# Kernel tuning notes

Measured on AMD Instinct MI355X. Metric: run time of the kernel, lower is better.

## Reference

```python
import jax, jax.numpy as jnp
import numpy as np

NUM_FEATURE = 50


def setup_inputs() -> dict:
    key = jax.random.key(0)
    k1, k2 = jax.random.split(key)
    query = jax.random.normal(k1, (512, NUM_FEATURE), dtype=jnp.float32)
    doc = jax.random.normal(k2, (512, 256, NUM_FEATURE), dtype=jnp.float32)
    # nn.Linear(150, 1, bias=False) with weight filled with 1
    W = jnp.ones((3 * NUM_FEATURE,), dtype=jnp.float32)
    return {"query": query, "doc": doc, "W": W}


def reference(query, doc, W):
    # Split the single 150-dim linear weight into the three trilinear parts:
    # score(x, y) = w1.sen_x + w2.q_y + w3.(sen_x * q_y)
    w1, w2, w3 = W[:NUM_FEATURE], W[NUM_FEATURE:2 * NUM_FEATURE], W[2 * NUM_FEATURE:]
    q_term = query @ w2                      # [Lq]
    qw3 = query * w3                         # [Lq, d]

    def per_sentence(sen):                   # sen: [Ls, d]
        sXY = (sen @ w1)[:, None] + q_term[None, :] + sen @ qw3.T   # [Ls, Lq]
        sD2Q = jax.nn.softmax(sXY, axis=0)   # softmax over sentence tokens
        sQ2D = jax.nn.softmax(sXY, axis=1)   # softmax over query tokens
        aD2Q = sD2Q @ query                  # [Ls, d]
        aQ2D = sD2Q @ (sQ2D.T @ sen)         # (sD2Q @ sQ2D.T) @ sen, cheaper order
        return jnp.concatenate([sen, aD2Q, sen * aD2Q, sen * aQ2D], axis=1)  # [Ls, 4d]

    return jax.vmap(per_sentence)(doc)       # [n_sen, Ls, 4d]
```

## Files before the change

### kernel.cpp

```cpp
#include <hip/hip_runtime.h>
#include <math.h>

typedef __bf16 bf16_t;
typedef bf16_t bf16x2 __attribute__((ext_vector_type(2)));
typedef bf16_t bf16x4 __attribute__((ext_vector_type(4)));
typedef bf16_t bf16x8 __attribute__((ext_vector_type(8)));
typedef float f32x4 __attribute__((ext_vector_type(4)));

#define MFMA16(a,b,c) __builtin_amdgcn_mfma_f32_16x16x32_bf16((a),(b),(c),0,0,0)

#define ND 256
#define NQ 512
#define NF 50
#define L2E 1.44269504f
#define SHIFT 64.0f

#define SENT_E 0
#define PD_E   13728
#define PQ_E   23968
#define QW3_E  32416
#define QTT_E  34720
#define GT_E   36800
#define SEN72_E 13728
#define P1Q_E  13728
#define PART_B 77760
#define QTB_B  78784
#define RINV_B 79808
#define LDS_BYTES 80832

__launch_bounds__(512, 4)
__global__ void ca15_kernel(const float* __restrict__ query,
                            const float* __restrict__ doc,
                            const float* __restrict__ W,
                            float* __restrict__ out)
{
    extern __shared__ char smem[];
    bf16_t* lb = (bf16_t*)smem;
    float*  part  = (float*)(smem + PART_B);
    bf16_t* qtb   = (bf16_t*)(smem + QTB_B);
    float*  rinvf = (float*)(smem + RINV_B);

    const int tid = threadIdx.x;
    const int w = tid >> 6, l = tid & 63, ln = l & 15, lg = l >> 4;
    const int s = blockIdx.x;
    const float* sen_g = doc + (size_t)s * (ND * NF);
    const bf16x4 z4 = (bf16x4){(bf16_t)0.f,(bf16_t)0.f,(bf16_t)0.f,(bf16_t)0.f};

    auto stage_p1 = [&](int jt, int buf) {
        const int j0 = jt * 64;
        bf16_t* dst = lb + P1Q_E + buf * 4608;
        for (int e = tid; e < 1664; e += 512) {
            int jj = e / 26, c = e - jj * 26;
            if (c < 25) {
                float2 v = ((const float2*)query)[(j0 + jj) * 25 + c];
                bf16x2 p;
                p[0] = (bf16_t)(v.x * W[100 + 2 * c] * L2E);
                p[1] = (bf16_t)(v.y * W[100 + 2 * c + 1] * L2E);
                *(bf16x2*)&dst[jj * 72 + 2 * c] = p;
            } else {
                bf16x2 p;
                p[0] = (bf16_t)((float)qtb[j0 + jj] * L2E);
                p[1] = (bf16_t)L2E;
                *(bf16x2*)&dst[jj * 72 + 50] = p;
            }
        }
    };
    auto stage_qw3 = [&](int jt) {
        const int j0 = jt * 32;
        bf16_t* dst = lb + QW3_E;
        for (int e = tid; e < 832; e += 512) {
            int jj = e / 26, c = e - jj * 26;
            if (c < 25) {
                float2 v = ((const float2*)query)[(j0 + jj) * 25 + c];
                bf16x2 p;
                p[0] = (bf16_t)(v.x * W[100 + 2 * c] * L2E);
                p[1] = (bf16_t)(v.y * W[100 + 2 * c + 1] * L2E);
                *(bf16x2*)&dst[jj * 72 + 2 * c] = p;
            } else {
                bf16x2 p;
                p[0] = (bf16_t)((float)qtb[j0 + jj] * L2E);
                p[1] = (bf16_t)L2E;
                *(bf16x2*)&dst[jj * 72 + 50] = p;
            }
        }
    };
    auto stage_qtt = [&](int jt) {
        const int j0 = jt * 32;
        for (int e = tid; e < 800; e += 512) {
            int c = e >> 5, jj = e & 31;
            float2 v = ((const float2*)query)[(j0 + jj) * 25 + c];
            lb[QTT_E + (2 * c) * 40 + jj]     = (bf16_t)v.x;
            lb[QTT_E + (2 * c + 1) * 40 + jj] = (bf16_t)v.y;
        }
    };

    for (int e = tid; e < 132; e += 512) {
        int f = 50 + e / 66, c4 = (e - (e / 66) * 66) * 4;
        *(bf16x4*)&lb[SENT_E + f * 264 + c4] = z4;
    }
    for (int e = tid; e < 768; e += 512) {
        int i = e / 3, c4 = 52 + (e - (e / 3) * 3) * 4;
        *(bf16x4*)&lb[SEN72_E + i * 72 + c4] = z4;
    }
    for (int e = tid; e < 6400; e += 512) {
        int i = e / 25, c = e - (e / 25) * 25;
        float2 v = ((const float2*)sen_g)[i * 25 + c];
        bf16x2 p; p[0] = (bf16_t)v.x; p[1] = (bf16_t)v.y;
        *(bf16x2*)&lb[SEN72_E + i * 72 + 2 * c] = p;
        lb[SENT_E + (2 * c) * 264 + i]     = p[0];
        lb[SENT_E + (2 * c + 1) * 264 + i] = p[1];
    }
    {
        float acc = 0.f;
        #pragma unroll
        for (int c = 0; c < 25; ++c) {
            float2 v = ((const float2*)query)[tid * 25 + c];
            acc += v.x * W[NF + 2 * c] + v.y * W[NF + 2 * c + 1];
        }
        qtb[tid] = (bf16_t)acc;
    }
    if (tid < ND) {
        float acc = 0.f;
        #pragma unroll
        for (int c = 0; c < 25; ++c) {
            float2 v = ((const float2*)sen_g)[tid * 25 + c];
            acc += v.x * W[2 * c] + v.y * W[2 * c + 1];
        }
        lb[SEN72_E + tid * 72 + 50] = (bf16_t)1.0f;
        lb[SEN72_E + tid * 72 + 51] = (bf16_t)acc;
    }
    __syncthreads();

    bf16x8 aS[2][2];
    #pragma unroll
    for (int mf = 0; mf < 2; ++mf)
        #pragma unroll
        for (int ks = 0; ks < 2; ++ks)
            aS[mf][ks] = *(bf16x8*)&lb[SEN72_E + (w * 32 + mf * 16 + ln) * 72 + lg * 8 + ks * 32];
    __syncthreads();

    for (int e = tid; e < 384; e += 512) {
        int buf = e / 192, r = e - buf * 192;
        int jj = r / 3, c4 = 52 + (r - (r / 3) * 3) * 4;
        *(bf16x4*)&lb[P1Q_E + buf * 4608 + jj * 72 + c4] = z4;
    }
    stage_p1(0, 0);
    __syncthreads();

    float rpart[2][4] = {{0.f,0.f,0.f,0.f},{0.f,0.f,0.f,0.f}};
    for (int jt = 0; jt < 8; ++jt) {
        if (jt < 7) stage_p1(jt + 1, (jt + 1) & 1);
        const bf16_t* qb = lb + P1Q_E + (jt & 1) * 4608;
        f32x4 sacc[2][4];
        #pragma unroll
        for (int mf = 0; mf < 2; ++mf)
            #pragma unroll
            for (int nf = 0; nf < 4; ++nf)
                sacc[mf][nf] = (f32x4){-SHIFT, -SHIFT, -SHIFT, -SHIFT};
        #pragma unroll
        for (int ks = 0; ks < 2; ++ks)
            #pragma unroll
            for (int nf = 0; nf < 4; ++nf) {
                bf16x8 b = *(bf16x8*)&qb[(nf * 16 + ln) * 72 + lg * 8 + ks * 32];
                sacc[0][nf] = MFMA16(aS[0][ks], b, sacc[0][nf]);
                sacc[1][nf] = MFMA16(aS[1][ks], b, sacc[1][nf]);
            }
        #pragma unroll
        for (int mf = 0; mf < 2; ++mf)
            #pragma unroll
            for (int nf = 0; nf < 4; ++nf)
                #pragma unroll
                for (int r = 0; r < 4; ++r)
                    rpart[mf][r] += exp2f(sacc[mf][nf][r]);
        __syncthreads();
    }
    #pragma unroll
    for (int mf = 0; mf < 2; ++mf)
        #pragma unroll
        for (int r = 0; r < 4; ++r) {
            float v = rpart[mf][r];
            v += __shfl_xor(v, 1);
            v += __shfl_xor(v, 2);
            v += __shfl_xor(v, 4);
            v += __shfl_xor(v, 8);
            if (ln == 0) rinvf[w * 32 + mf * 16 + lg * 4 + r] = 1.f / v;
        }
    __syncthreads();
    for (int e = tid; e < 12800; e += 512) {
        int f = e / 256, i = e & 255;
        lb[SENT_E + f * 264 + i] = (bf16_t)((float)lb[SENT_E + f * 264 + i] * rinvf[i]);
    }
    for (int e = tid; e < 96; e += 512) {
        int jj = e / 3, c4 = 52 + (e - (e / 3) * 3) * 4;
        *(bf16x4*)&lb[QW3_E + jj * 72 + c4] = z4;
    }
    stage_qw3(0);
    __syncthreads();

    f32x4 accD[2][4], accQ[2][4];
    #pragma unroll
    for (int mf = 0; mf < 2; ++mf)
        #pragma unroll
        for (int nf = 0; nf < 4; ++nf) {
            accD[mf][nf] = (f32x4){0.f, 0.f, 0.f, 0.f};
            accQ[mf][nf] = (f32x4){0.f, 0.f, 0.f, 0.f};
        }
    bf16x8 aPs[2];
    const int jf = w & 1, ff = w >> 1;
    int qtt_row[4], gt_row[4];
    #pragma unroll
    for (int nf = 0; nf < 4; ++nf) {
        int f = nf * 16 + ln;
        int rc = f < 51 ? f : 51;
        qtt_row[nf] = QTT_E + rc * 40;
        gt_row[nf]  = GT_E + rc * 40;
    }
    const int fg = ff * 16 + ln;
    const int sent_row = SENT_E + (fg < 51 ? fg : 51) * 264;

    for (int jt = 0; jt < 16; ++jt) {
        if (jt > 0) {
            #pragma unroll
            for (int nf = 0; nf < 4; ++nf) {
                bf16x8 bg = *(bf16x8*)&lb[gt_row[nf] + lg * 8];
                accQ[0][nf] = MFMA16(aPs[0], bg, accQ[0][nf]);
                accQ[1][nf] = MFMA16(aPs[1], bg, accQ[1][nf]);
            }
        }
        f32x4 sacc[2][2];
        #pragma unroll
        for (int mf = 0; mf < 2; ++mf)
            #pragma unroll
            for (int n2 = 0; n2 < 2; ++n2)
                sacc[mf][n2] = (f32x4){-SHIFT, -SHIFT, -SHIFT, -SHIFT};
        #pragma unroll
        for (int ks = 0; ks < 2; ++ks)
            #pragma unroll
            for (int n2 = 0; n2 < 2; ++n2) {
                bf16x8 b = *(bf16x8*)&lb[QW3_E + (n2 * 16 + ln) * 72 + lg * 8 + ks * 32];
                sacc[0][n2] = MFMA16(aS[0][ks], b, sacc[0][n2]);
                sacc[1][n2] = MFMA16(aS[1][ks], b, sacc[1][n2]);
            }
        #pragma unroll
        for (int n2 = 0; n2 < 2; ++n2) {
            #pragma unroll
            for (int mf = 0; mf < 2; ++mf)
                #pragma unroll
                for (int r = 0; r < 4; ++r)
                    sacc[mf][n2][r] = exp2f(sacc[mf][n2][r]);
            float cp = ((sacc[0][n2][0] + sacc[0][n2][1]) + (sacc[0][n2][2] + sacc[0][n2][3]))
                     + ((sacc[1][n2][0] + sacc[1][n2][1]) + (sacc[1][n2][2] + sacc[1][n2][3]));
            cp += __shfl_xor(cp, 16);
            cp += __shfl_xor(cp, 32);
            if (lg == 0) part[w * 32 + n2 * 16 + ln] = cp;
            #pragma unroll
            for (int mf = 0; mf < 2; ++mf) {
                bf16x4 pk;
                #pragma unroll
                for (int r = 0; r < 4; ++r) pk[r] = (bf16_t)sacc[mf][n2][r];
                *(bf16x4*)&lb[PQ_E + (n2 * 16 + ln) * 264 + w * 32 + mf * 16 + lg * 4] = pk;
                #pragma unroll
                for (int r = 0; r < 4; ++r)
                    lb[PD_E + (w * 32 + mf * 16 + lg * 4 + r) * 40 + n2 * 16 + ln] = pk[r];
            }
        }
        stage_qtt(jt);
        __syncthreads();

        float cs = 0.f;
        #pragma unroll
        for (int ww = 0; ww < 8; ++ww) cs += part[ww * 32 + (l & 31)];
        float civ = 1.f / cs;
        float cv[8];
        #pragma unroll
        for (int e = 0; e < 8; ++e) cv[e] = __shfl(civ, lg * 8 + e);
        #pragma unroll
        for (int mf = 0; mf < 2; ++mf) {
            bf16x8 raw = *(bf16x8*)&lb[PD_E + (w * 32 + mf * 16 + ln) * 40 + lg * 8];
            #pragma unroll
            for (int e = 0; e < 8; ++e)
                aPs[mf][e] = (bf16_t)((float)raw[e] * cv[e]);
        }
        #pragma unroll
        for (int nf = 0; nf < 4; ++nf) {
            bf16x8 bq = *(bf16x8*)&lb[qtt_row[nf] + lg * 8];
            accD[0][nf] = MFMA16(aPs[0], bq, accD[0][nf]);
            accD[1][nf] = MFMA16(aPs[1], bq, accD[1][nf]);
        }
        {
            f32x4 g = (f32x4){0.f, 0.f, 0.f, 0.f};
            #pragma unroll
            for (int ks = 0; ks < 8; ++ks) {
                bf16x8 a = *(bf16x8*)&lb[PQ_E + (jf * 16 + ln) * 264 + ks * 32 + lg * 8];
                bf16x8 b = *(bf16x8*)&lb[sent_row + ks * 32 + lg * 8];
                g = MFMA16(a, b, g);
            }
            if (fg < 52) {
                bf16x4 gk;
                #pragma unroll
                for (int r = 0; r < 4; ++r) gk[r] = (bf16_t)g[r];
                *(bf16x4*)&lb[GT_E + fg * 40 + jf * 16 + lg * 4] = gk;
            }
        }
        if (jt < 15) stage_qw3(jt + 1);
        __syncthreads();
    }
    #pragma unroll
    for (int nf = 0; nf < 4; ++nf) {
        bf16x8 bg = *(bf16x8*)&lb[gt_row[nf] + lg * 8];
        accQ[0][nf] = MFMA16(aPs[0], bg, accQ[0][nf]);
        accQ[1][nf] = MFMA16(aPs[1], bg, accQ[1][nf]);
    }
    __syncthreads();

    float* ea = (float*)smem;
    #pragma unroll
    for (int mf = 0; mf < 2; ++mf)
        #pragma unroll
        for (int nf = 0; nf < 4; ++nf) {
            int f = nf * 16 + ln;
            if (f < 56)
                #pragma unroll
                for (int r = 0; r < 4; ++r)
                    ea[(w * 32 + mf * 16 + lg * 4 + r) * 56 + f] = accD[mf][nf][r];
        }
    __syncthreads();
    const size_t ob0 = (size_t)s * (ND * 200);
    for (int v = tid; v < 6400; v += 512) {
        int i = v / 25, c = v - (v / 25) * 25, f = 2 * c;
        *(float2*)&out[ob0 + (size_t)i * 200 + f] = *(const float2*)&sen_g[i * 50 + f];
    }
    for (int v = tid; v < 6400; v += 512) {
        int i = v / 25, c = v - (v / 25) * 25, f = 2 * c;
        float2 o;
        o.x = ea[i * 56 + f]; o.y = ea[i * 56 + f + 1];
        *(float2*)&out[ob0 + (size_t)i * 200 + 50 + f] = o;
    }
    for (int v = tid; v < 6400; v += 512) {
        int i = v / 25, c = v - (v / 25) * 25, f = 2 * c;
        float2 d = *(const float2*)&sen_g[i * 50 + f];
        float2 o;
        o.x = d.x * ea[i * 56 + f]; o.y = d.y * ea[i * 56 + f + 1];
        *(float2*)&out[ob0 + (size_t)i * 200 + 100 + f] = o;
    }
    __syncthreads();
    #pragma unroll
    for (int mf = 0; mf < 2; ++mf)
        #pragma unroll
        for (int nf = 0; nf < 4; ++nf) {
            int f = nf * 16 + ln;
            if (f < 56)
                #pragma unroll
                for (int r = 0; r < 4; ++r)
                    ea[(w * 32 + mf * 16 + lg * 4 + r) * 56 + f] = accQ[mf][nf][r];
        }
    __syncthreads();
    for (int v = tid; v < 6400; v += 512) {
        int i = v / 25, c = v - (v / 25) * 25, f = 2 * c;
        float2 d = *(const float2*)&sen_g[i * 50 + f];
        float2 o;
        o.x = d.x * ea[i * 56 + f]; o.y = d.y * ea[i * 56 + f + 1];
        *(float2*)&out[ob0 + (size_t)i * 200 + 150 + f] = o;
    }
}

extern "C" void kernel_launch(void* const* d_in, const int* in_sizes, int n_in,
                              void* d_out, int out_size, void* d_ws, size_t ws_size,
                              hipStream_t stream) {
    const float* query = (const float*)d_in[0];
    const float* doc   = (const float*)d_in[1];
    const float* W     = (const float*)d_in[2];
    float* out = (float*)d_out;
    (void)d_ws; (void)ws_size; (void)n_in; (void)in_sizes; (void)out_size;

    hipFuncSetAttribute((const void*)ca15_kernel,
                        hipFuncAttributeMaxDynamicSharedMemorySize,
                        LDS_BYTES);
    ca15_kernel<<<dim3(512), dim3(512), LDS_BYTES, stream>>>(query, doc, W, out);
}
```

Baseline: 147.4 us.

## Merge aD2Q and aQ2D accumulations into one combined B operand matrix

The query tile and the G^T tile now sit in one LDS buffer (QG), so a single loop of seven MFMA column fragments per step accumulates both the D2Q and the Q2D outputs. Previously two separate four-fragment loops did this. The shared A operand is reused, so seven fragments replace eight and one loop with its LDS reads goes away. Row strides change from 72/40 to 76/36, which cuts LDS size slightly and alters bank-conflict patterns. The query-tile staging also moves after the G computation, and the accumulator register count shrinks, which may help occupancy.

```diff
diff --git a/kernel.cpp b/kernel.cpp
--- a/kernel.cpp
+++ b/kernel.cpp
@@ -16,20 +16,19 @@
 #define SHIFT 64.0f
 
 #define SENT_E 0
-#define PD_E   13728
-#define PQ_E   23968
-#define QW3_E  32416
-#define QTT_E  34720
-#define GT_E   36800
+#define QW3_E  13728
+#define QG_E   16160
+#define PD_E   20192
+#define PQ_E   29408
 #define SEN72_E 13728
 #define P1Q_E  13728
-#define PART_B 77760
-#define QTB_B  78784
-#define RINV_B 79808
-#define LDS_BYTES 80832
+#define PART_B 75712
+#define QTB_B  76736
+#define RINV_B 77760
+#define LDS_BYTES 78784
 
 __launch_bounds__(512, 4)
-__global__ void ca15_kernel(const float* __restrict__ query,
+__global__ void ca16_kernel(const float* __restrict__ query,
                             const float* __restrict__ doc,
                             const float* __restrict__ W,
                             float* __restrict__ out)
@@ -48,7 +47,7 @@
 
     auto stage_p1 = [&](int jt, int buf) {
         const int j0 = jt * 64;
-        bf16_t* dst = lb + P1Q_E + buf * 4608;
+        bf16_t* dst = lb + P1Q_E + buf * 4864;
         for (int e = tid; e < 1664; e += 512) {
             int jj = e / 26, c = e - jj * 26;
             if (c < 25) {
@@ -56,18 +55,17 @@
                 bf16x2 p;
                 p[0] = (bf16_t)(v.x * W[100 + 2 * c] * L2E);
                 p[1] = (bf16_t)(v.y * W[100 + 2 * c + 1] * L2E);
-                *(bf16x2*)&dst[jj * 72 + 2 * c] = p;
+                *(bf16x2*)&dst[jj * 76 + 2 * c] = p;
             } else {
                 bf16x2 p;
                 p[0] = (bf16_t)((float)qtb[j0 + jj] * L2E);
                 p[1] = (bf16_t)L2E;
-                *(bf16x2*)&dst[jj * 72 + 50] = p;
+                *(bf16x2*)&dst[jj * 76 + 50] = p;
             }
         }
     };
     auto stage_qw3 = [&](int jt) {
         const int j0 = jt * 32;
-        bf16_t* dst = lb + QW3_E;
         for (int e = tid; e < 832; e += 512) {
             int jj = e / 26, c = e - jj * 26;
             if (c < 25) {
@@ -75,22 +73,22 @@
                 bf16x2 p;
                 p[0] = (bf16_t)(v.x * W[100 + 2 * c] * L2E);
                 p[1] = (bf16_t)(v.y * W[100 + 2 * c + 1] * L2E);
-                *(bf16x2*)&dst[jj * 72 + 2 * c] = p;
+                *(bf16x2*)&lb[QW3_E + jj * 76 + 2 * c] = p;
             } else {
                 bf16x2 p;
                 p[0] = (bf16_t)((float)qtb[j0 + jj] * L2E);
                 p[1] = (bf16_t)L2E;
-                *(bf16x2*)&dst[jj * 72 + 50] = p;
+                *(bf16x2*)&lb[QW3_E + jj * 76 + 50] = p;
             }
         }
     };
-    auto stage_qtt = [&](int jt) {
+    auto stage_qgq = [&](int jt) {
         const int j0 = jt * 32;
         for (int e = tid; e < 800; e += 512) {
             int c = e >> 5, jj = e & 31;
             float2 v = ((const float2*)query)[(j0 + jj) * 25 + c];
-            lb[QTT_E + (2 * c) * 40 + jj]     = (bf16_t)v.x;
-            lb[QTT_E + (2 * c + 1) * 40 + jj] = (bf16_t)v.y;
+            lb[QG_E + (2 * c) * 36 + jj]     = (bf16_t)v.x;
+            lb[QG_E + (2 * c + 1) * 36 + jj] = (bf16_t)v.y;
         }
     };
 
@@ -98,8 +96,8 @@
         int f = 50 + e / 66, c4 = (e - (e / 66) * 66) * 4;
         *(bf16x4*)&lb[SENT_E + f * 264 + c4] = z4;
     }
-    for (int e = tid; e < 768; e += 512) {
-        int i = e / 3, c4 = 52 + (e - (e / 3) * 3) * 4;
+    for (int e = tid; e < 1280; e += 512) {
+        int i = e / 5, c4 = 52 + (e - (e / 5) * 5) * 4;
         *(bf16x4*)&lb[SEN72_E + i * 72 + c4] = z4;
     }
     for (int e = tid; e < 6400; e += 512) {
@@ -142,7 +140,7 @@
     for (int e = tid; e < 384; e += 512) {
         int buf = e / 192, r = e - buf * 192;
         int jj = r / 3, c4 = 52 + (r - (r / 3) * 3) * 4;
-        *(bf16x4*)&lb[P1Q_E + buf * 4608 + jj * 72 + c4] = z4;
+        *(bf16x4*)&lb[P1Q_E + buf * 4864 + jj * 76 + c4] = z4;
     }
     stage_p1(0, 0);
     __syncthreads();
@@ -150,7 +148,7 @@
     float rpart[2][4] = {{0.f,0.f,0.f,0.f},{0.f,0.f,0.f,0.f}};
     for (int jt = 0; jt < 8; ++jt) {
         if (jt < 7) stage_p1(jt + 1, (jt + 1) & 1);
-        const bf16_t* qb = lb + P1Q_E + (jt & 1) * 4608;
+        const bf16_t* qb = lb + P1Q_E + (jt & 1) * 4864;
         f32x4 sacc[2][4];
         #pragma unroll
         for (int mf = 0; mf < 2; ++mf)
@@ -161,7 +159,7 @@
         for (int ks = 0; ks < 2; ++ks)
             #pragma unroll
             for (int nf = 0; nf < 4; ++nf) {
-                bf16x8 b = *(bf16x8*)&qb[(nf * 16 + ln) * 72 + lg * 8 + ks * 32];
+                bf16x8 b = *(bf16x8*)&qb[(nf * 16 + ln) * 76 + lg * 8 + ks * 32];
                 sacc[0][nf] = MFMA16(aS[0][ks], b, sacc[0][nf]);
                 sacc[1][nf] = MFMA16(aS[1][ks], b, sacc[1][nf]);
             }
@@ -186,70 +184,60 @@
             if (ln == 0) rinvf[w * 32 + mf * 16 + lg * 4 + r] = 1.f / v;
         }
     __syncthreads();
+
     for (int e = tid; e < 12800; e += 512) {
         int f = e / 256, i = e & 255;
         lb[SENT_E + f * 264 + i] = (bf16_t)((float)lb[SENT_E + f * 264 + i] * rinvf[i]);
     }
     for (int e = tid; e < 96; e += 512) {
         int jj = e / 3, c4 = 52 + (e - (e / 3) * 3) * 4;
-        *(bf16x4*)&lb[QW3_E + jj * 72 + c4] = z4;
+        *(bf16x4*)&lb[QW3_E + jj * 76 + c4] = z4;
+    }
+    for (int e = tid; e < 108; e += 512) {
+        int rr = e / 9, c4 = (e - (e / 9) * 9) * 4;
+        int row = (rr < 2) ? (50 + rr) : (100 + rr);
+        *(bf16x4*)&lb[QG_E + row * 36 + c4] = z4;
     }
     stage_qw3(0);
     __syncthreads();
 
-    f32x4 accD[2][4], accQ[2][4];
-    #pragma unroll
-    for (int mf = 0; mf < 2; ++mf)
-        #pragma unroll
-        for (int nf = 0; nf < 4; ++nf) {
-            accD[mf][nf] = (f32x4){0.f, 0.f, 0.f, 0.f};
-            accQ[mf][nf] = (f32x4){0.f, 0.f, 0.f, 0.f};
-        }
+    f32x4 accQG[2][7];
+    #pragma unroll
+    for (int mf = 0; mf < 2; ++mf)
+        #pragma unroll
+        for (int nf = 0; nf < 7; ++nf) accQG[mf][nf] = (f32x4){0.f, 0.f, 0.f, 0.f};
     bf16x8 aPs[2];
     const int jf = w & 1, ff = w >> 1;
-    int qtt_row[4], gt_row[4];
-    #pragma unroll
-    for (int nf = 0; nf < 4; ++nf) {
-        int f = nf * 16 + ln;
-        int rc = f < 51 ? f : 51;
-        qtt_row[nf] = QTT_E + rc * 40;
-        gt_row[nf]  = GT_E + rc * 40;
-    }
     const int fg = ff * 16 + ln;
     const int sent_row = SENT_E + (fg < 51 ? fg : 51) * 264;
 
     for (int jt = 0; jt < 16; ++jt) {
         if (jt > 0) {
             #pragma unroll
-            for (int nf = 0; nf < 4; ++nf) {
-                bf16x8 bg = *(bf16x8*)&lb[gt_row[nf] + lg * 8];
-                accQ[0][nf] = MFMA16(aPs[0], bg, accQ[0][nf]);
-                accQ[1][nf] = MFMA16(aPs[1], bg, accQ[1][nf]);
-            }
-        }
-        f32x4 sacc[2][2];
-        #pragma unroll
-        for (int mf = 0; mf < 2; ++mf)
-            #pragma unroll
-            for (int n2 = 0; n2 < 2; ++n2)
-                sacc[mf][n2] = (f32x4){-SHIFT, -SHIFT, -SHIFT, -SHIFT};
-        #pragma unroll
-        for (int ks = 0; ks < 2; ++ks)
-            #pragma unroll
-            for (int n2 = 0; n2 < 2; ++n2) {
-                bf16x8 b = *(bf16x8*)&lb[QW3_E + (n2 * 16 + ln) * 72 + lg * 8 + ks * 32];
-                sacc[0][n2] = MFMA16(aS[0][ks], b, sacc[0][n2]);
-                sacc[1][n2] = MFMA16(aS[1][ks], b, sacc[1][n2]);
-            }
+            for (int nf = 0; nf < 7; ++nf) {
+                bf16x8 b = *(bf16x8*)&lb[QG_E + (nf * 16 + ln) * 36 + lg * 8];
+                accQG[0][nf] = MFMA16(aPs[0], b, accQG[0][nf]);
+                accQG[1][nf] = MFMA16(aPs[1], b, accQG[1][nf]);
+            }
+        }
         #pragma unroll
         for (int n2 = 0; n2 < 2; ++n2) {
+            f32x4 sacc[2];
+            sacc[0] = (f32x4){-SHIFT, -SHIFT, -SHIFT, -SHIFT};
+            sacc[1] = (f32x4){-SHIFT, -SHIFT, -SHIFT, -SHIFT};
+            #pragma unroll
+            for (int ks = 0; ks < 2; ++ks) {
+                bf16x8 b = *(bf16x8*)&lb[QW3_E + (n2 * 16 + ln) * 76 + lg * 8 + ks * 32];
+                sacc[0] = MFMA16(aS[0][ks], b, sacc[0]);
+                sacc[1] = MFMA16(aS[1][ks], b, sacc[1]);
+            }
             #pragma unroll
             for (int mf = 0; mf < 2; ++mf)
                 #pragma unroll
                 for (int r = 0; r < 4; ++r)
-                    sacc[mf][n2][r] = exp2f(sacc[mf][n2][r]);
-            float cp = ((sacc[0][n2][0] + sacc[0][n2][1]) + (sacc[0][n2][2] + sacc[0][n2][3]))
-                     + ((sacc[1][n2][0] + sacc[1][n2][1]) + (sacc[1][n2][2] + sacc[1][n2][3]));
+                    sacc[mf][r] = exp2f(sacc[mf][r]);
+            float cp = ((sacc[0][0] + sacc[0][1]) + (sacc[0][2] + sacc[0][3]))
+                     + ((sacc[1][0] + sacc[1][1]) + (sacc[1][2] + sacc[1][3]));
             cp += __shfl_xor(cp, 16);
             cp += __shfl_xor(cp, 32);
             if (lg == 0) part[w * 32 + n2 * 16 + ln] = cp;
@@ -257,14 +245,13 @@
             for (int mf = 0; mf < 2; ++mf) {
                 bf16x4 pk;
                 #pragma unroll
-                for (int r = 0; r < 4; ++r) pk[r] = (bf16_t)sacc[mf][n2][r];
+                for (int r = 0; r < 4; ++r) pk[r] = (bf16_t)sacc[mf][r];
                 *(bf16x4*)&lb[PQ_E + (n2 * 16 + ln) * 264 + w * 32 + mf * 16 + lg * 4] = pk;
                 #pragma unroll
                 for (int r = 0; r < 4; ++r)
-                    lb[PD_E + (w * 32 + mf * 16 + lg * 4 + r) * 40 + n2 * 16 + ln] = pk[r];
-            }
-        }
-        stage_qtt(jt);
+                    lb[PD_E + (w * 32 + mf * 16 + lg * 4 + r) * 36 + n2 * 16 + ln] = pk[r];
+            }
+        }
         __syncthreads();
 
         float cs = 0.f;
@@ -276,16 +263,10 @@
         for (int e = 0; e < 8; ++e) cv[e] = __shfl(civ, lg * 8 + e);
         #pragma unroll
         for (int mf = 0; mf < 2; ++mf) {
-            bf16x8 raw = *(bf16x8*)&lb[PD_E + (w * 32 + mf * 16 + ln) * 40 + lg * 8];
+            bf16x8 raw = *(bf16x8*)&lb[PD_E + (w * 32 + mf * 16 + ln) * 36 + lg * 8];
             #pragma unroll
             for (int e = 0; e < 8; ++e)
                 aPs[mf][e] = (bf16_t)((float)raw[e] * cv[e]);
-        }
-        #pragma unroll
-        for (int nf = 0; nf < 4; ++nf) {
-            bf16x8 bq = *(bf16x8*)&lb[qtt_row[nf] + lg * 8];
-            accD[0][nf] = MFMA16(aPs[0], bq, accD[0][nf]);
-            accD[1][nf] = MFMA16(aPs[1], bq, accD[1][nf]);
         }
         {
             f32x4 g = (f32x4){0.f, 0.f, 0.f, 0.f};
@@ -299,17 +280,18 @@
                 bf16x4 gk;
                 #pragma unroll
                 for (int r = 0; r < 4; ++r) gk[r] = (bf16_t)g[r];
-                *(bf16x4*)&lb[GT_E + fg * 40 + jf * 16 + lg * 4] = gk;
-            }
-        }
+                *(bf16x4*)&lb[QG_E + (52 + fg) * 36 + jf * 16 + lg * 4] = gk;
+            }
+        }
+        stage_qgq(jt);
         if (jt < 15) stage_qw3(jt + 1);
         __syncthreads();
     }
     #pragma unroll
-    for (int nf = 0; nf < 4; ++nf) {
-        bf16x8 bg = *(bf16x8*)&lb[gt_row[nf] + lg * 8];
-        accQ[0][nf] = MFMA16(aPs[0], bg, accQ[0][nf]);
-        accQ[1][nf] = MFMA16(aPs[1], bg, accQ[1][nf]);
+    for (int nf = 0; nf < 7; ++nf) {
+        bf16x8 b = *(bf16x8*)&lb[QG_E + (nf * 16 + ln) * 36 + lg * 8];
+        accQG[0][nf] = MFMA16(aPs[0], b, accQG[0][nf]);
+        accQG[1][nf] = MFMA16(aPs[1], b, accQG[1][nf]);
     }
     __syncthreads();
 
@@ -319,10 +301,10 @@
         #pragma unroll
         for (int nf = 0; nf < 4; ++nf) {
             int f = nf * 16 + ln;
-            if (f < 56)
-                #pragma unroll
-                for (int r = 0; r < 4; ++r)
-                    ea[(w * 32 + mf * 16 + lg * 4 + r) * 56 + f] = accD[mf][nf][r];
+            if (f < 50)
+                #pragma unroll
+                for (int r = 0; r < 4; ++r)
+                    ea[(w * 32 + mf * 16 + lg * 4 + r) * 56 + f] = accQG[mf][nf][r];
         }
     __syncthreads();
     const size_t ob0 = (size_t)s * (ND * 200);
@@ -347,12 +329,12 @@
     #pragma unroll
     for (int mf = 0; mf < 2; ++mf)
         #pragma unroll
-        for (int nf = 0; nf < 4; ++nf) {
-            int f = nf * 16 + ln;
-            if (f < 56)
-                #pragma unroll
-                for (int r = 0; r < 4; ++r)
-                    ea[(w * 32 + mf * 16 + lg * 4 + r) * 56 + f] = accQ[mf][nf][r];
+        for (int nf = 3; nf < 7; ++nf) {
+            int qf = nf * 16 + ln - 52;
+            if (qf >= 0 && qf < 50)
+                #pragma unroll
+                for (int r = 0; r < 4; ++r)
+                    ea[(w * 32 + mf * 16 + lg * 4 + r) * 56 + qf] = accQG[mf][nf][r];
         }
     __syncthreads();
     for (int v = tid; v < 6400; v += 512) {
@@ -373,8 +355,8 @@
     float* out = (float*)d_out;
     (void)d_ws; (void)ws_size; (void)n_in; (void)in_sizes; (void)out_size;
 
-    hipFuncSetAttribute((const void*)ca15_kernel,
+    hipFuncSetAttribute((const void*)ca16_kernel,
                         hipFuncAttributeMaxDynamicSharedMemorySize,
                         LDS_BYTES);
-    ca15_kernel<<<dim3(512), dim3(512), LDS_BYTES, stream>>>(query, doc, W, out);
+    ca16_kernel<<<dim3(512), dim3(512), LDS_BYTES, stream>>>(query, doc, W, out);
 }
```

Measured after the change: 216.0 us. +46.6%, slower.
